# Kernel optimization log

Hardware: AMD Instinct MI355X
Metric: run time of the kernel (lower is better)

Reference implementation:

```python
import jax, jax.numpy as jnp
import numpy as np

IN_DIM = 256
OUT_DIM = 256
NUM = 5        # grid_size
K = 3          # spline_order
GRID_RANGE = (-1.0, 1.0)


def extend_grid(grid, k_extend):
    # grid: (in_dim, num+1) -> (in_dim, num+1+2*k_extend)
    h = (grid[:, -1:] - grid[:, :1]) / (grid.shape[1] - 1)
    for _ in range(k_extend):
        grid = jnp.concatenate([grid[:, :1] - h, grid, grid[:, -1:] + h], axis=1)
    return grid


def b_spline_basis(x, grid, k):
    # x: (B, in_dim), grid: (in_dim, G). Cox-de Boor recursion, vectorized.
    x = x[:, :, None]                 # (B, in, 1)
    g = grid[None, :, :]              # (1, in, G)
    B = ((x >= g[:, :, :-1]) & (x < g[:, :, 1:])).astype(x.dtype)  # order 0
    for p in range(1, k + 1):
        left = (x - g[:, :, :-(p + 1)]) / (g[:, :, p:-1] - g[:, :, :-(p + 1)])
        right = (g[:, :, p + 1:] - x) / (g[:, :, p + 1:] - g[:, :, 1:-p])
        B = left * B[:, :, :-1] + right * B[:, :, 1:]
    return jnp.nan_to_num(B)          # (B, in, num+k)


def setup_inputs() -> dict:
    key = jax.random.key(0)
    kx, kc, kb, ks = jax.random.split(key, 4)
    x = jax.random.uniform(kx, (2048, IN_DIM), dtype=jnp.float32,
                           minval=GRID_RANGE[0], maxval=GRID_RANGE[1])
    base_grid = jnp.broadcast_to(
        jnp.linspace(GRID_RANGE[0], GRID_RANGE[1], NUM + 1, dtype=jnp.float32)[None, :],
        (IN_DIM, NUM + 1))
    grid = extend_grid(base_grid, K)                        # (in, num+1+2k)
    coef = 0.1 * jax.random.normal(kc, (IN_DIM, OUT_DIM, NUM + K), dtype=jnp.float32)
    scale_base = ((jax.random.uniform(kb, (IN_DIM, OUT_DIM), dtype=jnp.float32) * 2 - 1)
                  / np.sqrt(IN_DIM).astype(np.float32))
    scale_sp = jnp.ones((IN_DIM, OUT_DIM), dtype=jnp.float32)
    mask = jnp.ones((IN_DIM, OUT_DIM), dtype=jnp.float32)
    return {"x": x, "grid": grid, "coef": coef,
            "scale_base": scale_base, "scale_sp": scale_sp, "mask": mask}


def reference(x, grid, coef, scale_base, scale_sp, mask):
    base = jax.nn.silu(x)                                   # (B, in)
    B = b_spline_basis(x, grid, K)                          # (B, in, num+k)
    # coef2curve: (B, in, G) x (in, out, G) -> (B, in, out)
    y = jnp.einsum('big,iog->bio', B, coef)
    y = scale_base[None, :, :] * base[:, :, None] + scale_sp[None, :, :] * y
    y = mask[None, :, :] * y
    return jnp.sum(y, axis=1)                               # (B, out)
```

## Files before the change

### kernel.cpp

```cpp
#include <hip/hip_runtime.h>

#define BATCH 2048
#define IND   256
#define OUTD  256

typedef __attribute__((ext_vector_type(8))) short bf16x8;
typedef __attribute__((ext_vector_type(4))) float f32x4;

__device__ __forceinline__ ushort f2bf(float f) {
    uint u = __builtin_bit_cast(uint, f);
    u += 0x7fffu + ((u >> 16) & 1u);
    return (ushort)(u >> 16);
}
__device__ __forceinline__ uint pack2(float lo, float hi) {
    return (uint)f2bf(lo) | ((uint)f2bf(hi) << 16);
}

#define BIASOFF (1u << 20)
#define FOFF    ((1u << 20) + 4096)
#define WS_NEED ((size_t)FOFF + (size_t)IND * BATCH * 16)

__device__ __forceinline__ uint4 feat_pack(float xv) {
    const float u = (xv + 1.0f) * 2.5f;
    float cif = floorf(u);
    cif = fminf(fmaxf(cif, 0.0f), 4.0f);
    const int ci = (int)cif;
    const float f = u - cif, mf = 1.0f - f;
    const float f2 = f * f, f3 = f2 * f;
    const float k6 = 1.0f / 6.0f;
    const float w0 = mf * mf * mf * k6;
    const float w1 = (3.0f * f3 - 6.0f * f2 + 4.0f) * k6;
    const float w3 = f3 * k6;
    const float w2 = 1.0f - w0 - w1 - w3;
    const float sg = __fdividef(xv, 1.0f + __expf(-xv));
    const float B0 = (ci == 0) ? w0 : 0.f;
    const float B1 = (ci == 1) ? w0 : (ci == 0) ? w1 : 0.f;
    const float B2 = (ci == 2) ? w0 : (ci == 1) ? w1 : (ci == 0) ? w2 : 0.f;
    const float B3 = (ci == 3) ? w0 : (ci == 2) ? w1 : (ci == 1) ? w2 : (ci == 0) ? w3 : 0.f;
    const float B4 = (ci == 4) ? w0 : (ci == 3) ? w1 : (ci == 2) ? w2 : (ci == 1) ? w3 : 0.f;
    const float B5 = (ci == 4) ? w1 : (ci == 3) ? w2 : (ci == 2) ? w3 : 0.f;
    const float B6 = (ci == 4) ? w2 : (ci == 3) ? w3 : 0.f;
    uint4 v;
    v.x = pack2(sg, B0); v.y = pack2(B1, B2);
    v.z = pack2(B3, B4); v.w = pack2(B5, B6);
    return v;
}

__global__ __launch_bounds__(256) void kan_prep(
    const float* __restrict__ x, const float* __restrict__ coef,
    const float* __restrict__ sb, const float* __restrict__ ss,
    const float* __restrict__ mask,
    uint4* __restrict__ W, float* __restrict__ bias, uint4* __restrict__ F)
{
    const int bid = blockIdx.x, tid = threadIdx.x;
    __shared__ float xt[4 * 260];
    __shared__ float part[32][8];

    const int b0 = bid * 4;
    {
        const int row = tid >> 6, c4 = (tid & 63) * 4;
        const float4 v = *reinterpret_cast<const float4*>(
            x + (size_t)(b0 + row) * IND + c4);
        xt[row * 260 + c4 + 0] = v.x;
        xt[row * 260 + c4 + 1] = v.y;
        xt[row * 260 + c4 + 2] = v.z;
        xt[row * 260 + c4 + 3] = v.w;
    }

    if (tid < 128) {
        const int i = bid >> 1, o = (bid & 1) * 128 + tid;
        const int io = i * OUTD + o;
        const float m = mask[io], b = sb[io], sp = ss[io];
        const float4* cp = reinterpret_cast<const float4*>(coef + (size_t)io * 8);
        const float4 c0 = cp[0], c1 = cp[1];
        const float wb = m * b, wsp = m * sp;
        const float c7 = c1.w;
        uint4 w;
        w.x = pack2(wb,                wsp * (c0.x - c7));
        w.y = pack2(wsp * (c0.y - c7), wsp * (c0.z - c7));
        w.z = pack2(wsp * (c0.w - c7), wsp * (c1.x - c7));
        w.w = pack2(wsp * (c1.y - c7), wsp * (c1.z - c7));
        W[io] = w;
    }
    __syncthreads();

#pragma unroll
    for (int p = 0; p < 4; ++p) {
        const int q = p * 256 + tid;
        const int i = q >> 2, b = q & 3;
        F[(size_t)i * BATCH + b0 + b] = feat_pack(xt[b * 260 + i]);
    }

    if (bid >= 480) {
        const int o0 = (bid - 480) * 8;
        const int ol = tid & 7, ig = tid >> 3;
        float s = 0.f;
#pragma unroll
        for (int ii = 0; ii < 8; ++ii) {
            const int i = ig * 8 + ii;
            const int io = i * OUTD + o0 + ol;
            s += mask[io] * ss[io] * coef[(size_t)io * 8 + 7];
        }
        part[ig][ol] = s;
        __syncthreads();
        if (tid < 8) {
            float acc = 0.f;
#pragma unroll
            for (int g2 = 0; g2 < 32; ++g2) acc += part[g2][tid];
            bias[o0 + tid] = acc;
        }
    }
}

__global__ __launch_bounds__(1024, 4) void kan_gemm(
    const uint4* __restrict__ F, const uint4* __restrict__ W,
    const float* __restrict__ bias, float* __restrict__ out)
{
    const int tid  = threadIdx.x;
    const int lane = tid & 63, wid = tid >> 6;
    const int nh = wid & 1, kq = wid >> 1;
    const int r = lane & 15, g = lane >> 4;
    const int b0 = (blockIdx.x >> 2) * 32;
    const int o0 = (blockIdx.x & 3) * 64;

    const uint4* pA = F + (size_t)(kq * 32 + g) * BATCH + b0 + r;
    const uint4* pB = W + (size_t)(kq * 32 + g) * OUTD + o0 + nh * 32 + r;

    f32x4 acc[2][2] = {};
    bf16x8 aC0, aC1, bC0, bC1, aN0, aN1, bN0, bN1;

#define LD(A0, A1, B0_, B1_, t)                                                        \
    {                                                                                  \
        A0  = *reinterpret_cast<const bf16x8*>(pA + (size_t)(4 * (t)) * BATCH);        \
        A1  = *reinterpret_cast<const bf16x8*>(pA + (size_t)(4 * (t)) * BATCH + 16);   \
        B0_ = *reinterpret_cast<const bf16x8*>(pB + (size_t)(4 * (t)) * OUTD);         \
        B1_ = *reinterpret_cast<const bf16x8*>(pB + (size_t)(4 * (t)) * OUTD + 16);    \
    }
#define MM(A0, A1, B0_, B1_)                                                           \
    {                                                                                  \
        acc[0][0] = __builtin_amdgcn_mfma_f32_16x16x32_bf16(A0, B0_, acc[0][0], 0, 0, 0); \
        acc[0][1] = __builtin_amdgcn_mfma_f32_16x16x32_bf16(A0, B1_, acc[0][1], 0, 0, 0); \
        acc[1][0] = __builtin_amdgcn_mfma_f32_16x16x32_bf16(A1, B0_, acc[1][0], 0, 0, 0); \
        acc[1][1] = __builtin_amdgcn_mfma_f32_16x16x32_bf16(A1, B1_, acc[1][1], 0, 0, 0); \
    }

    LD(aC0, aC1, bC0, bC1, 0);
#pragma unroll
    for (int t = 0; t < 8; t += 2) {
        if (t + 1 < 8) LD(aN0, aN1, bN0, bN1, t + 1);
        MM(aC0, aC1, bC0, bC1);
        if (t + 2 < 8) LD(aC0, aC1, bC0, bC1, t + 2);
        if (t + 1 < 8) MM(aN0, aN1, bN0, bN1);
    }
#undef LD
#undef MM

    __shared__ float red[2][7][1024];
    if (kq > 0) {
        float* dst = &red[nh][kq - 1][0];
#pragma unroll
        for (int mf = 0; mf < 2; ++mf)
#pragma unroll
            for (int nf = 0; nf < 2; ++nf)
                *reinterpret_cast<f32x4*>(dst + (mf * 2 + nf) * 256 + lane * 4) = acc[mf][nf];
    }
    __syncthreads();
    if (kq == 0) {
#pragma unroll
        for (int mf = 0; mf < 2; ++mf)
#pragma unroll
            for (int nf = 0; nf < 2; ++nf) {
                f32x4 s = acc[mf][nf];
                const int sl = (mf * 2 + nf) * 256 + lane * 4;
#pragma unroll
                for (int kk = 0; kk < 7; ++kk) {
                    const f32x4 v = *reinterpret_cast<const f32x4*>(&red[nh][kk][0] + sl);
                    s.x += v.x; s.y += v.y; s.z += v.z; s.w += v.w;
                }
                const int col  = o0 + nh * 32 + nf * 16 + r;
                const int row0 = b0 + mf * 16 + g * 4;
                const float bv = bias[col];
#pragma unroll
                for (int e = 0; e < 4; ++e)
                    out[(size_t)(row0 + e) * OUTD + col] = s[e] + bv;
            }
    }
}

#define KPI  16
#define IPC  8
#define KC   (IPC * KPI)

__global__ __launch_bounds__(256, 2) void kan_mfma(
    const float* __restrict__ x, const float* __restrict__ coef,
    const float* __restrict__ scale_base, const float* __restrict__ scale_sp,
    const float* __restrict__ mask, float* __restrict__ out)
{
    const int tid = threadIdx.x;
    const int b0 = blockIdx.x * 32, o0 = blockIdx.y * 32;
    __shared__ uint Fa[32 * KC / 2];
    __shared__ uint Wt2[32 * KC / 2];
    for (int j = tid; j < 32 * KC / 2; j += 256) { Fa[j] = 0u; Wt2[j] = 0u; }
    const int lane = tid & 63, wid = tid >> 6;
    const int wmv = (wid >> 1) * 16, wnv = (wid & 1) * 16;
    f32x4 acc = {0.f, 0.f, 0.f, 0.f};
    const int fb = tid & 31, il = tid >> 5;
    for (int ic = 0; ic < IND / IPC; ++ic) {
        const int i = ic * IPC + il;
        __syncthreads();
        {
            const uint4 fp = feat_pack(x[(b0 + fb) * IND + i]);
            const int base = fb * (KC / 2) + il * (KPI / 2);
            const int sw = (fb & 7) << 2;
            Fa[(base + 0) ^ sw] = fp.x; Fa[(base + 1) ^ sw] = fp.y;
            Fa[(base + 2) ^ sw] = fp.z; Fa[(base + 3) ^ sw] = fp.w;
            ((ushort*)Fa)[2 * ((base + 4) ^ sw)] = 0;
        }
        {
            const int io = i * OUTD + o0 + fb;
            const float m = mask[io];
            const float wb = scale_base[io] * m, wsv = scale_sp[io] * m;
            const float4* cp = reinterpret_cast<const float4*>(coef + (size_t)io * 8);
            const float4 c0 = cp[0], c1 = cp[1];
            const float c7 = c1.w;
            const int base = fb * (KC / 2) + il * (KPI / 2);
            const int sw = (fb & 7) << 2;
            Wt2[(base + 0) ^ sw] = pack2(wb, wsv * (c0.x - c7));
            Wt2[(base + 1) ^ sw] = pack2(wsv * (c0.y - c7), wsv * (c0.z - c7));
            Wt2[(base + 2) ^ sw] = pack2(wsv * (c0.w - c7), wsv * (c1.x - c7));
            Wt2[(base + 3) ^ sw] = pack2(wsv * (c1.y - c7), wsv * (c1.z - c7));
            ((ushort*)Wt2)[2 * ((base + 4) ^ sw)] = 0;
        }
        __syncthreads();
        {
            const ushort* fs = (const ushort*)Fa;
            const ushort* wsd = (const ushort*)Wt2;
            const int ar = wmv + (lane & 15), br = wnv + (lane & 15);
            const int kg = (lane >> 4) * 8;
#pragma unroll
            for (int ksi = 0; ksi < 4; ++ksi) {
                const int ka = ksi * 32 + kg;
                const int ia = (ar * KC + ka) ^ ((ar & 7) << 3);
                const int ib = (br * KC + ka) ^ ((br & 7) << 3);
                bf16x8 a = *reinterpret_cast<const bf16x8*>(fs + ia);
                bf16x8 b = *reinterpret_cast<const bf16x8*>(wsd + ib);
                acc = __builtin_amdgcn_mfma_f32_16x16x32_bf16(a, b, acc, 0, 0, 0);
            }
        }
    }
    const int col = o0 + wnv + (lane & 15);
    const int row0 = b0 + wmv + ((lane >> 4) << 2);
    float bv = 0.f;
    for (int i = 0; i < IND; ++i) {
        const int io = i * OUTD + col;
        bv += mask[io] * scale_sp[io] * coef[(size_t)io * 8 + 7];
    }
#pragma unroll
    for (int rr = 0; rr < 4; ++rr)
        out[(size_t)(row0 + rr) * OUTD + col] = acc[rr] + bv;
}

extern "C" void kernel_launch(void* const* d_in, const int* in_sizes, int n_in,
                              void* d_out, int out_size, void* d_ws, size_t ws_size,
                              hipStream_t stream) {
    const float* x          = (const float*)d_in[0];
    const float* coef       = (const float*)d_in[2];
    const float* scale_base = (const float*)d_in[3];
    const float* scale_sp   = (const float*)d_in[4];
    const float* mask       = (const float*)d_in[5];
    float* out = (float*)d_out;

    if (ws_size >= WS_NEED) {
        uint4* W    = (uint4*)d_ws;
        float* bias = (float*)((char*)d_ws + BIASOFF);
        uint4* F    = (uint4*)((char*)d_ws + FOFF);
        kan_prep<<<512, 256, 0, stream>>>(x, coef, scale_base, scale_sp, mask, W, bias, F);
        kan_gemm<<<256, 1024, 0, stream>>>(F, W, bias, out);
    } else {
        kan_mfma<<<dim3(BATCH / 32, OUTD / 32), 256, 0, stream>>>(
            x, coef, scale_base, scale_sp, mask, out);
    }
}
```

Measured before the change: 21.23 us.

## Stage GEMM operands through LDS with direct global-to-LDS loads and swizzle

Transposes the feature and weight workspaces to row-major K-contiguous layouts and rewrites the GEMM to stage 64x32 A tiles and 32x32 W tiles into double-buffered shared memory using global_load_lds with an XOR swizzle. Block tiles change to 64 batch rows by 32 outputs with a remapped block index. The goal is coalesced, reusable operand loads instead of per-wave strided global reads. It adds a barrier per K step and 96KB of LDS per block, which limits occupancy to one block per CU.

```diff
diff --git a/kernel.cpp b/kernel.cpp
--- a/kernel.cpp
+++ b/kernel.cpp
@@ -6,6 +6,9 @@
 
 typedef __attribute__((ext_vector_type(8))) short bf16x8;
 typedef __attribute__((ext_vector_type(4))) float f32x4;
+
+#define AS1 __attribute__((address_space(1)))
+#define AS3 __attribute__((address_space(3)))
 
 __device__ __forceinline__ ushort f2bf(float f) {
     uint u = __builtin_bit_cast(uint, f);
@@ -50,7 +53,7 @@
     const float* __restrict__ x, const float* __restrict__ coef,
     const float* __restrict__ sb, const float* __restrict__ ss,
     const float* __restrict__ mask,
-    uint4* __restrict__ W, float* __restrict__ bias, uint4* __restrict__ F)
+    uint4* __restrict__ WT, float* __restrict__ bias, uint4* __restrict__ F)
 {
     const int bid = blockIdx.x, tid = threadIdx.x;
     __shared__ float xt[4 * 260];
@@ -80,16 +83,13 @@
         w.y = pack2(wsp * (c0.y - c7), wsp * (c0.z - c7));
         w.z = pack2(wsp * (c0.w - c7), wsp * (c1.x - c7));
         w.w = pack2(wsp * (c1.y - c7), wsp * (c1.z - c7));
-        W[io] = w;
+        WT[(size_t)o * IND + i] = w;
     }
     __syncthreads();
 
 #pragma unroll
-    for (int p = 0; p < 4; ++p) {
-        const int q = p * 256 + tid;
-        const int i = q >> 2, b = q & 3;
-        F[(size_t)i * BATCH + b0 + b] = feat_pack(xt[b * 260 + i]);
-    }
+    for (int p = 0; p < 4; ++p)
+        F[(size_t)(b0 + p) * IND + tid] = feat_pack(xt[p * 260 + tid]);
 
     if (bid >= 480) {
         const int o0 = (bid - 480) * 8;
@@ -112,52 +112,75 @@
     }
 }
 
-__global__ __launch_bounds__(1024, 4) void kan_gemm(
-    const uint4* __restrict__ F, const uint4* __restrict__ W,
+__global__ __launch_bounds__(1024, 1) void kan_gemm(
+    const uint4* __restrict__ F, const uint4* __restrict__ WT,
     const float* __restrict__ bias, float* __restrict__ out)
 {
+    __shared__ uint4 smem[6144];
+
     const int tid  = threadIdx.x;
     const int lane = tid & 63, wid = tid >> 6;
-    const int nh = wid & 1, kq = wid >> 1;
+    const int wm = wid & 1, ks = wid >> 1;
     const int r = lane & 15, g = lane >> 4;
-    const int b0 = (blockIdx.x >> 2) * 32;
-    const int o0 = (blockIdx.x & 3) * 64;
-
-    const uint4* pA = F + (size_t)(kq * 32 + g) * BATCH + b0 + r;
-    const uint4* pB = W + (size_t)(kq * 32 + g) * OUTD + o0 + nh * 32 + r;
+    const int bid = blockIdx.x;
+    const int b0 = (((bid & 7) << 2) + (bid >> 6)) * 64;
+    const int o0 = ((bid >> 3) & 7) * 32;
+
+    const int s0 = wid * 128 + lane;
+    const int s1 = s0 + 64;
+    const int rA0 = s0 >> 5, cA0 = (s0 & 31) ^ (rA0 & 7);
+    const int rA1 = s1 >> 5, cA1 = (s1 & 31) ^ (rA1 & 7);
+    const int s2 = wid * 64 + lane;
+    const int rW = s2 >> 5, cW = (s2 & 31) ^ (rW & 7);
+    const uint4* pA0 = F  + (size_t)(b0 + rA0) * IND + cA0;
+    const uint4* pA1 = F  + (size_t)(b0 + rA1) * IND + cA1;
+    const uint4* pW  = WT + (size_t)(o0 + rW) * IND + cW;
+
+    int aoff[2], woff[2];
+#pragma unroll
+    for (int mr = 0; mr < 2; ++mr) {
+        const int arow = wm * 32 + mr * 16 + r;
+        aoff[mr] = arow * 32 + ((ks * 4 + g) ^ (arow & 7));
+    }
+#pragma unroll
+    for (int nr = 0; nr < 2; ++nr) {
+        const int orow = nr * 16 + r;
+        woff[nr] = orow * 32 + ((ks * 4 + g) ^ (orow & 7));
+    }
 
     f32x4 acc[2][2] = {};
-    bf16x8 aC0, aC1, bC0, bC1, aN0, aN1, bN0, bN1;
-
-#define LD(A0, A1, B0_, B1_, t)                                                        \
-    {                                                                                  \
-        A0  = *reinterpret_cast<const bf16x8*>(pA + (size_t)(4 * (t)) * BATCH);        \
-        A1  = *reinterpret_cast<const bf16x8*>(pA + (size_t)(4 * (t)) * BATCH + 16);   \
-        B0_ = *reinterpret_cast<const bf16x8*>(pB + (size_t)(4 * (t)) * OUTD);         \
-        B1_ = *reinterpret_cast<const bf16x8*>(pB + (size_t)(4 * (t)) * OUTD + 16);    \
-    }
-#define MM(A0, A1, B0_, B1_)                                                           \
-    {                                                                                  \
-        acc[0][0] = __builtin_amdgcn_mfma_f32_16x16x32_bf16(A0, B0_, acc[0][0], 0, 0, 0); \
-        acc[0][1] = __builtin_amdgcn_mfma_f32_16x16x32_bf16(A0, B1_, acc[0][1], 0, 0, 0); \
-        acc[1][0] = __builtin_amdgcn_mfma_f32_16x16x32_bf16(A1, B0_, acc[1][0], 0, 0, 0); \
-        acc[1][1] = __builtin_amdgcn_mfma_f32_16x16x32_bf16(A1, B1_, acc[1][1], 0, 0, 0); \
-    }
-
-    LD(aC0, aC1, bC0, bC1, 0);
-#pragma unroll
-    for (int t = 0; t < 8; t += 2) {
-        if (t + 1 < 8) LD(aN0, aN1, bN0, bN1, t + 1);
-        MM(aC0, aC1, bC0, bC1);
-        if (t + 2 < 8) LD(aC0, aC1, bC0, bC1, t + 2);
-        if (t + 1 < 8) MM(aN0, aN1, bN0, bN1);
-    }
-#undef LD
-#undef MM
-
-    __shared__ float red[2][7][1024];
-    if (kq > 0) {
-        float* dst = &red[nh][kq - 1][0];
+
+#define STAGE(t, buf)                                                              \
+    {                                                                              \
+        __builtin_amdgcn_global_load_lds((const AS1 uint*)(pA0 + (size_t)(t) * 32),\
+            (AS3 uint*)(smem + (buf) * 2048 + wid * 128), 16, 0, 0);               \
+        __builtin_amdgcn_global_load_lds((const AS1 uint*)(pA1 + (size_t)(t) * 32),\
+            (AS3 uint*)(smem + (buf) * 2048 + wid * 128 + 64), 16, 0, 0);          \
+        __builtin_amdgcn_global_load_lds((const AS1 uint*)(pW  + (size_t)(t) * 32),\
+            (AS3 uint*)(smem + 4096 + (buf) * 1024 + wid * 64), 16, 0, 0);         \
+    }
+
+    STAGE(0, 0);
+    for (int t = 0; t < 8; ++t) {
+        __syncthreads();
+        if (t < 7) STAGE(t + 1, (t + 1) & 1);
+        const uint4* Ab = smem + (t & 1) * 2048;
+        const uint4* Wb = smem + 4096 + (t & 1) * 1024;
+        bf16x8 a0 = *reinterpret_cast<const bf16x8*>(Ab + aoff[0]);
+        bf16x8 a1 = *reinterpret_cast<const bf16x8*>(Ab + aoff[1]);
+        bf16x8 w0 = *reinterpret_cast<const bf16x8*>(Wb + woff[0]);
+        bf16x8 w1 = *reinterpret_cast<const bf16x8*>(Wb + woff[1]);
+        acc[0][0] = __builtin_amdgcn_mfma_f32_16x16x32_bf16(a0, w0, acc[0][0], 0, 0, 0);
+        acc[0][1] = __builtin_amdgcn_mfma_f32_16x16x32_bf16(a0, w1, acc[0][1], 0, 0, 0);
+        acc[1][0] = __builtin_amdgcn_mfma_f32_16x16x32_bf16(a1, w0, acc[1][0], 0, 0, 0);
+        acc[1][1] = __builtin_amdgcn_mfma_f32_16x16x32_bf16(a1, w1, acc[1][1], 0, 0, 0);
+    }
+#undef STAGE
+
+    __syncthreads();
+    float* red = (float*)smem;
+    if (ks > 0) {
+        float* dst = red + (size_t)(wm * 7 + ks - 1) * 1024;
 #pragma unroll
         for (int mf = 0; mf < 2; ++mf)
 #pragma unroll
@@ -165,7 +188,7 @@
                 *reinterpret_cast<f32x4*>(dst + (mf * 2 + nf) * 256 + lane * 4) = acc[mf][nf];
     }
     __syncthreads();
-    if (kq == 0) {
+    if (ks == 0) {
 #pragma unroll
         for (int mf = 0; mf < 2; ++mf)
 #pragma unroll
@@ -174,11 +197,12 @@
                 const int sl = (mf * 2 + nf) * 256 + lane * 4;
 #pragma unroll
                 for (int kk = 0; kk < 7; ++kk) {
-                    const f32x4 v = *reinterpret_cast<const f32x4*>(&red[nh][kk][0] + sl);
+                    const f32x4 v = *reinterpret_cast<const f32x4*>(
+                        red + (size_t)(wm * 7 + kk) * 1024 + sl);
                     s.x += v.x; s.y += v.y; s.z += v.z; s.w += v.w;
                 }
-                const int col  = o0 + nh * 32 + nf * 16 + r;
-                const int row0 = b0 + mf * 16 + g * 4;
+                const int col  = o0 + nf * 16 + r;
+                const int row0 = b0 + wm * 32 + mf * 16 + g * 4;
                 const float bv = bias[col];
 #pragma unroll
                 for (int e = 0; e < 4; ++e)
@@ -271,11 +295,11 @@
     float* out = (float*)d_out;
 
     if (ws_size >= WS_NEED) {
-        uint4* W    = (uint4*)d_ws;
+        uint4* WT   = (uint4*)d_ws;
         float* bias = (float*)((char*)d_ws + BIASOFF);
         uint4* F    = (uint4*)((char*)d_ws + FOFF);
-        kan_prep<<<512, 256, 0, stream>>>(x, coef, scale_base, scale_sp, mask, W, bias, F);
-        kan_gemm<<<256, 1024, 0, stream>>>(F, W, bias, out);
+        kan_prep<<<512, 256, 0, stream>>>(x, coef, scale_base, scale_sp, mask, WT, bias, F);
+        kan_gemm<<<256, 1024, 0, stream>>>(F, WT, bias, out);
     } else {
         kan_mfma<<<dim3(BATCH / 32, OUTD / 32), 256, 0, stream>>>(
             x, coef, scale_base, scale_sp, mask, out);
```

New measurement: 23.69 us. 11.6% more time.

## Fuse prep and GEMM into one cooperative kernel with grid sync

Applied to the files above, without the earlier changes.

Merges the feature/weight packing kernel and the bf16 MFMA GEMM kernel into a single cooperative launch of 256 blocks, separated by a grid-wide barrier, to remove one kernel launch and its inter-kernel gap. Blocks are mapped by XCD so each block's GEMM tile rows match the batch rows it packed, which may improve L2 locality. The old two-kernel path stays as a fallback if the cooperative launch fails. Risks include grid sync overhead and lower occupancy flexibility with 1024-thread blocks.

```diff
diff --git a/kernel.cpp b/kernel.cpp
--- a/kernel.cpp
+++ b/kernel.cpp
@@ -1,4 +1,7 @@
 #include <hip/hip_runtime.h>
+#include <hip/hip_cooperative_groups.h>
+
+namespace cg = cooperative_groups;
 
 #define BATCH 2048
 #define IND   256
@@ -46,6 +49,145 @@
     return v;
 }
 
+__global__ __launch_bounds__(1024, 4) void kan_one(
+    const float* __restrict__ x, const float* __restrict__ coef,
+    const float* __restrict__ sb, const float* __restrict__ ss,
+    const float* __restrict__ mask,
+    uint4* __restrict__ W, float* __restrict__ bias, uint4* __restrict__ F,
+    float* __restrict__ out)
+{
+    __shared__ float shm[2 * 7 * 1024];
+
+    const int bid = blockIdx.x, tid = threadIdx.x;
+    const int xcd = bid & 7;
+
+    {
+        const int b0p = xcd * 256 + (bid >> 3) * 8;
+        float* xs = shm;
+        {
+            const int row = tid >> 7, c2 = (tid & 127) * 2;
+            const float2 v = *reinterpret_cast<const float2*>(
+                x + (size_t)(b0p + row) * IND + c2);
+            xs[row * 258 + c2]     = v.x;
+            xs[row * 258 + c2 + 1] = v.y;
+        }
+        if (tid < 256) {
+            const int io = bid * OUTD + tid;
+            const float m = mask[io], b = sb[io], sp = ss[io];
+            const float4* cp = reinterpret_cast<const float4*>(coef + (size_t)io * 8);
+            const float4 c0 = cp[0], c1 = cp[1];
+            const float wb = m * b, wsp = m * sp;
+            const float c7 = c1.w;
+            uint4 w;
+            w.x = pack2(wb,                wsp * (c0.x - c7));
+            w.y = pack2(wsp * (c0.y - c7), wsp * (c0.z - c7));
+            w.z = pack2(wsp * (c0.w - c7), wsp * (c1.x - c7));
+            w.w = pack2(wsp * (c1.y - c7), wsp * (c1.z - c7));
+            W[io] = w;
+        }
+        __syncthreads();
+#pragma unroll
+        for (int p = 0; p < 2; ++p) {
+            const int q = p * 1024 + tid;
+            const int i = q >> 3, b = q & 7;
+            F[(size_t)i * BATCH + b0p + b] = feat_pack(xs[b * 258 + i]);
+        }
+        if (bid < 32 && tid < 256) {
+            float* part = shm + 2080;
+            const int o0b = bid * 8, ol = tid & 7, ig = tid >> 3;
+            float s = 0.f;
+#pragma unroll
+            for (int ii = 0; ii < 8; ++ii) {
+                const int i = ig * 8 + ii;
+                const int io = i * OUTD + o0b + ol;
+                s += mask[io] * ss[io] * coef[(size_t)io * 8 + 7];
+            }
+            part[ig * 8 + ol] = s;
+        }
+        __syncthreads();
+        if (bid < 32 && tid < 8) {
+            const float* part = shm + 2080;
+            float acc = 0.f;
+#pragma unroll
+            for (int g2 = 0; g2 < 32; ++g2) acc += part[g2 * 8 + tid];
+            bias[bid * 8 + tid] = acc;
+        }
+    }
+
+    cg::this_grid().sync();
+
+    const int lane = tid & 63, wid = tid >> 6;
+    const int nh = wid & 1, kq = wid >> 1;
+    const int r = lane & 15, g = lane >> 4;
+    const int b0 = xcd * 256 + ((bid >> 3) & 7) * 32;
+    const int o0 = (bid >> 6) * 64;
+
+    const uint4* pA = F + (size_t)(kq * 32 + g) * BATCH + b0 + r;
+    const uint4* pB = W + (size_t)(kq * 32 + g) * OUTD + o0 + nh * 32 + r;
+
+    f32x4 acc[2][2] = {};
+    bf16x8 aC0, aC1, bC0, bC1, aN0, aN1, bN0, bN1;
+
+#define LD(A0, A1, B0_, B1_, t)                                                        \
+    {                                                                                  \
+        A0  = *reinterpret_cast<const bf16x8*>(pA + (size_t)(4 * (t)) * BATCH);        \
+        A1  = *reinterpret_cast<const bf16x8*>(pA + (size_t)(4 * (t)) * BATCH + 16);   \
+        B0_ = *reinterpret_cast<const bf16x8*>(pB + (size_t)(4 * (t)) * OUTD);         \
+        B1_ = *reinterpret_cast<const bf16x8*>(pB + (size_t)(4 * (t)) * OUTD + 16);    \
+    }
+#define MM(A0, A1, B0_, B1_)                                                           \
+    {                                                                                  \
+        acc[0][0] = __builtin_amdgcn_mfma_f32_16x16x32_bf16(A0, B0_, acc[0][0], 0, 0, 0); \
+        acc[0][1] = __builtin_amdgcn_mfma_f32_16x16x32_bf16(A0, B1_, acc[0][1], 0, 0, 0); \
+        acc[1][0] = __builtin_amdgcn_mfma_f32_16x16x32_bf16(A1, B0_, acc[1][0], 0, 0, 0); \
+        acc[1][1] = __builtin_amdgcn_mfma_f32_16x16x32_bf16(A1, B1_, acc[1][1], 0, 0, 0); \
+    }
+
+    LD(aC0, aC1, bC0, bC1, 0);
+#pragma unroll
+    for (int t = 0; t < 8; t += 2) {
+        if (t + 1 < 8) LD(aN0, aN1, bN0, bN1, t + 1);
+        MM(aC0, aC1, bC0, bC1);
+        if (t + 2 < 8) LD(aC0, aC1, bC0, bC1, t + 2);
+        if (t + 1 < 8) MM(aN0, aN1, bN0, bN1);
+    }
+#undef LD
+#undef MM
+
+    __syncthreads();
+    float* red = shm;
+    if (kq > 0) {
+        float* dst = red + (size_t)(nh * 7 + kq - 1) * 1024;
+#pragma unroll
+        for (int mf = 0; mf < 2; ++mf)
+#pragma unroll
+            for (int nf = 0; nf < 2; ++nf)
+                *reinterpret_cast<f32x4*>(dst + (mf * 2 + nf) * 256 + lane * 4) = acc[mf][nf];
+    }
+    __syncthreads();
+    if (kq == 0) {
+#pragma unroll
+        for (int mf = 0; mf < 2; ++mf)
+#pragma unroll
+            for (int nf = 0; nf < 2; ++nf) {
+                f32x4 s = acc[mf][nf];
+                const int sl = (mf * 2 + nf) * 256 + lane * 4;
+#pragma unroll
+                for (int kk = 0; kk < 7; ++kk) {
+                    const f32x4 v = *reinterpret_cast<const f32x4*>(
+                        red + (size_t)(nh * 7 + kk) * 1024 + sl);
+                    s.x += v.x; s.y += v.y; s.z += v.z; s.w += v.w;
+                }
+                const int col  = o0 + nh * 32 + nf * 16 + r;
+                const int row0 = b0 + mf * 16 + g * 4;
+                const float bv = bias[col];
+#pragma unroll
+                for (int e = 0; e < 4; ++e)
+                    out[(size_t)(row0 + e) * OUTD + col] = s[e] + bv;
+            }
+    }
+}
+
 __global__ __launch_bounds__(256) void kan_prep(
     const float* __restrict__ x, const float* __restrict__ coef,
     const float* __restrict__ sb, const float* __restrict__ ss,
@@ -55,7 +197,6 @@
     const int bid = blockIdx.x, tid = threadIdx.x;
     __shared__ float xt[4 * 260];
     __shared__ float part[32][8];
-
     const int b0 = bid * 4;
     {
         const int row = tid >> 6, c4 = (tid & 63) * 4;
@@ -66,7 +207,6 @@
         xt[row * 260 + c4 + 2] = v.z;
         xt[row * 260 + c4 + 3] = v.w;
     }
-
     if (tid < 128) {
         const int i = bid >> 1, o = (bid & 1) * 128 + tid;
         const int io = i * OUTD + o;
@@ -83,14 +223,12 @@
         W[io] = w;
     }
     __syncthreads();
-
 #pragma unroll
     for (int p = 0; p < 4; ++p) {
         const int q = p * 256 + tid;
         const int i = q >> 2, b = q & 3;
         F[(size_t)i * BATCH + b0 + b] = feat_pack(xt[b * 260 + i]);
     }
-
     if (bid >= 480) {
         const int o0 = (bid - 480) * 8;
         const int ol = tid & 7, ig = tid >> 3;
@@ -274,8 +412,15 @@
         uint4* W    = (uint4*)d_ws;
         float* bias = (float*)((char*)d_ws + BIASOFF);
         uint4* F    = (uint4*)((char*)d_ws + FOFF);
-        kan_prep<<<512, 256, 0, stream>>>(x, coef, scale_base, scale_sp, mask, W, bias, F);
-        kan_gemm<<<256, 1024, 0, stream>>>(F, W, bias, out);
+
+        void* args[] = {(void*)&x, (void*)&coef, (void*)&scale_base, (void*)&scale_sp,
+                        (void*)&mask, (void*)&W, (void*)&bias, (void*)&F, (void*)&out};
+        hipError_t err = hipLaunchCooperativeKernel(
+            (const void*)kan_one, dim3(256), dim3(1024), args, 0, stream);
+        if (err != hipSuccess) {
+            kan_prep<<<512, 256, 0, stream>>>(x, coef, scale_base, scale_sp, mask, W, bias, F);
+            kan_gemm<<<256, 1024, 0, stream>>>(F, W, bias, out);
+        }
     } else {
         kan_mfma<<<dim3(BATCH / 32, OUTD / 32), 256, 0, stream>>>(
             x, coef, scale_base, scale_sp, mask, out);
```

New measurement: 55.20 us. 160% more time.

## Halve GEMM split-K waves, deepen register prefetch, and swizzle block-to-tile mapping

Applied to the files above, without the earlier changes.

The GEMM kernel now uses 8 waves per block instead of 16. Each wave covers 64 K-groups in place of 32, which shrinks the shared-memory split-K reduction from 7 partials to 3. A four-stage software register prefetch replaces the two-stage ping-pong. Block indices in both the prep and GEMM kernels are remapped so neighbouring block IDs land on different batch regions, aiming for better cache or XCD locality. The trade-off is a longer serial K loop per wave and more live registers in exchange for less reduction traffic and synchronisation.

```diff
diff --git a/kernel.cpp b/kernel.cpp
--- a/kernel.cpp
+++ b/kernel.cpp
@@ -56,7 +56,7 @@
     __shared__ float xt[4 * 260];
     __shared__ float part[32][8];
 
-    const int b0 = bid * 4;
+    const int b0 = (bid & 7) * 256 + (bid >> 3) * 4;
     {
         const int row = tid >> 6, c4 = (tid & 63) * 4;
         const float4 v = *reinterpret_cast<const float4*>(
@@ -112,7 +112,7 @@
     }
 }
 
-__global__ __launch_bounds__(1024, 4) void kan_gemm(
+__global__ __launch_bounds__(512, 4) void kan_gemm(
     const uint4* __restrict__ F, const uint4* __restrict__ W,
     const float* __restrict__ bias, float* __restrict__ out)
 {
@@ -120,42 +120,44 @@
     const int lane = tid & 63, wid = tid >> 6;
     const int nh = wid & 1, kq = wid >> 1;
     const int r = lane & 15, g = lane >> 4;
-    const int b0 = (blockIdx.x >> 2) * 32;
-    const int o0 = (blockIdx.x & 3) * 64;
-
-    const uint4* pA = F + (size_t)(kq * 32 + g) * BATCH + b0 + r;
-    const uint4* pB = W + (size_t)(kq * 32 + g) * OUTD + o0 + nh * 32 + r;
+    const int bid = blockIdx.x;
+    const int q = bid >> 3;
+    const int b0 = ((bid & 7) * 8 + (q >> 2)) * 32;
+    const int o0 = (q & 3) * 64;
+
+    const uint4* pA = F + (size_t)(kq * 64 + g) * BATCH + b0 + r;
+    const uint4* pB = W + (size_t)(kq * 64 + g) * OUTD + o0 + nh * 32 + r;
 
     f32x4 acc[2][2] = {};
-    bf16x8 aC0, aC1, bC0, bC1, aN0, aN1, bN0, bN1;
-
-#define LD(A0, A1, B0_, B1_, t)                                                        \
+    bf16x8 a0_0, a1_0, b0_0, b1_0;
+    bf16x8 a0_1, a1_1, b0_1, b1_1;
+    bf16x8 a0_2, a1_2, b0_2, b1_2;
+    bf16x8 a0_3, a1_3, b0_3, b1_3;
+
+#define LDS_(s, t)                                                                     \
     {                                                                                  \
-        A0  = *reinterpret_cast<const bf16x8*>(pA + (size_t)(4 * (t)) * BATCH);        \
-        A1  = *reinterpret_cast<const bf16x8*>(pA + (size_t)(4 * (t)) * BATCH + 16);   \
-        B0_ = *reinterpret_cast<const bf16x8*>(pB + (size_t)(4 * (t)) * OUTD);         \
-        B1_ = *reinterpret_cast<const bf16x8*>(pB + (size_t)(4 * (t)) * OUTD + 16);    \
-    }
-#define MM(A0, A1, B0_, B1_)                                                           \
+        a0_##s = *reinterpret_cast<const bf16x8*>(pA + (size_t)(4 * (t)) * BATCH);     \
+        a1_##s = *reinterpret_cast<const bf16x8*>(pA + (size_t)(4 * (t)) * BATCH + 16);\
+        b0_##s = *reinterpret_cast<const bf16x8*>(pB + (size_t)(4 * (t)) * OUTD);      \
+        b1_##s = *reinterpret_cast<const bf16x8*>(pB + (size_t)(4 * (t)) * OUTD + 16); \
+    }
+#define MM_(s)                                                                         \
     {                                                                                  \
-        acc[0][0] = __builtin_amdgcn_mfma_f32_16x16x32_bf16(A0, B0_, acc[0][0], 0, 0, 0); \
-        acc[0][1] = __builtin_amdgcn_mfma_f32_16x16x32_bf16(A0, B1_, acc[0][1], 0, 0, 0); \
-        acc[1][0] = __builtin_amdgcn_mfma_f32_16x16x32_bf16(A1, B0_, acc[1][0], 0, 0, 0); \
-        acc[1][1] = __builtin_amdgcn_mfma_f32_16x16x32_bf16(A1, B1_, acc[1][1], 0, 0, 0); \
-    }
-
-    LD(aC0, aC1, bC0, bC1, 0);
-#pragma unroll
-    for (int t = 0; t < 8; t += 2) {
-        if (t + 1 < 8) LD(aN0, aN1, bN0, bN1, t + 1);
-        MM(aC0, aC1, bC0, bC1);
-        if (t + 2 < 8) LD(aC0, aC1, bC0, bC1, t + 2);
-        if (t + 1 < 8) MM(aN0, aN1, bN0, bN1);
-    }
-#undef LD
-#undef MM
-
-    __shared__ float red[2][7][1024];
+        acc[0][0] = __builtin_amdgcn_mfma_f32_16x16x32_bf16(a0_##s, b0_##s, acc[0][0], 0, 0, 0); \
+        acc[0][1] = __builtin_amdgcn_mfma_f32_16x16x32_bf16(a0_##s, b1_##s, acc[0][1], 0, 0, 0); \
+        acc[1][0] = __builtin_amdgcn_mfma_f32_16x16x32_bf16(a1_##s, b0_##s, acc[1][0], 0, 0, 0); \
+        acc[1][1] = __builtin_amdgcn_mfma_f32_16x16x32_bf16(a1_##s, b1_##s, acc[1][1], 0, 0, 0); \
+    }
+
+    LDS_(0, 0)  LDS_(1, 1)  LDS_(2, 2)  LDS_(3, 3)
+    MM_(0) LDS_(0, 4)   MM_(1) LDS_(1, 5)   MM_(2) LDS_(2, 6)   MM_(3) LDS_(3, 7)
+    MM_(0) LDS_(0, 8)   MM_(1) LDS_(1, 9)   MM_(2) LDS_(2, 10)  MM_(3) LDS_(3, 11)
+    MM_(0) LDS_(0, 12)  MM_(1) LDS_(1, 13)  MM_(2) LDS_(2, 14)  MM_(3) LDS_(3, 15)
+    MM_(0) MM_(1) MM_(2) MM_(3)
+#undef LDS_
+#undef MM_
+
+    __shared__ float red[2][3][1024];
     if (kq > 0) {
         float* dst = &red[nh][kq - 1][0];
 #pragma unroll
@@ -173,7 +175,7 @@
                 f32x4 s = acc[mf][nf];
                 const int sl = (mf * 2 + nf) * 256 + lane * 4;
 #pragma unroll
-                for (int kk = 0; kk < 7; ++kk) {
+                for (int kk = 0; kk < 3; ++kk) {
                     const f32x4 v = *reinterpret_cast<const f32x4*>(&red[nh][kk][0] + sl);
                     s.x += v.x; s.y += v.y; s.z += v.z; s.w += v.w;
                 }
@@ -275,7 +277,7 @@
         float* bias = (float*)((char*)d_ws + BIASOFF);
         uint4* F    = (uint4*)((char*)d_ws + FOFF);
         kan_prep<<<512, 256, 0, stream>>>(x, coef, scale_base, scale_sp, mask, W, bias, F);
-        kan_gemm<<<256, 1024, 0, stream>>>(F, W, bias, out);
+        kan_gemm<<<256, 512, 0, stream>>>(F, W, bias, out);
     } else {
         kan_mfma<<<dim3(BATCH / 32, OUTD / 32), 256, 0, stream>>>(
             x, coef, scale_base, scale_sp, mask, out);
```

Result: faster. 18.27 us (-13.9%).
